# Kernel optimization log

Measured on AMD Instinct MI355X. Metric: run time of the kernel, lower is better.

The kernel has to match this reference:

```python
import jax, jax.numpy as jnp
import numpy as np

EMB_DIM = 1024
NUM_HEADS = 16
HEAD_DIM = EMB_DIM // NUM_HEADS


def setup_inputs() -> dict:
    key = jax.random.key(0)
    ks = jax.random.split(key, 10)
    B, Sq, Skv = 4, 4096, 4096
    scale = 1.0 / np.sqrt(EMB_DIM)
    inp = {
        "query": jax.random.normal(ks[0], (B, Sq, EMB_DIM), jnp.float32),
        "key_value": jax.random.normal(ks[1], (B, Skv, EMB_DIM), jnp.float32),
        "Wq": jax.random.normal(ks[2], (EMB_DIM, EMB_DIM), jnp.float32) * scale,
        "bq": jnp.zeros((EMB_DIM,), jnp.float32),
        "Wk": jax.random.normal(ks[3], (EMB_DIM, EMB_DIM), jnp.float32) * scale,
        "bk": jnp.zeros((EMB_DIM,), jnp.float32),
        "Wv": jax.random.normal(ks[4], (EMB_DIM, EMB_DIM), jnp.float32) * scale,
        "bv": jnp.zeros((EMB_DIM,), jnp.float32),
        "Wo": jax.random.normal(ks[5], (EMB_DIM, EMB_DIM), jnp.float32) * scale,
        "bo": jnp.zeros((EMB_DIM,), jnp.float32),
    }
    return inp


def reference(query, key_value, Wq, bq, Wk, bk, Wv, bv, Wo, bo):
    B, Sq, D = query.shape
    Skv = key_value.shape[1]
    H, hd = NUM_HEADS, HEAD_DIM
    # Projections -> [B, S, H, hd]
    Q = (query @ Wq + bq).reshape(B, Sq, H, hd)
    K = (key_value @ Wk + bk).reshape(B, Skv, H, hd)
    V = (key_value @ Wv + bv).reshape(B, Skv, H, hd)
    # elu+1 feature map (strictly positive)
    Q = jax.nn.elu(Q) + 1.0
    K = jax.nn.elu(K) + 1.0
    # KV summarization: [B, H, hd, hd]
    KV = jnp.einsum("bshd,bshe->bhde", K, V)
    K_sum = K.sum(axis=1)  # [B, H, hd]
    # Attention output and normalizer
    out = jnp.einsum("bqhd,bhde->bqhe", Q, KV)          # [B, Sq, H, hd]
    norm = jnp.einsum("bqhd,bhd->bqh", Q, K_sum)         # [B, Sq, H]
    out = out / (norm[..., None] + 1e-6)
    out = out.reshape(B, Sq, D)
    return out @ Wo + bo  # dropout is identity in eval
```

## Files before the change

kernel.cpp:

```cpp
#include <hip/hip_runtime.h>

typedef __bf16 bf16_t;
typedef __bf16 bf16x2 __attribute__((ext_vector_type(2)));
typedef __bf16 bf16x8 __attribute__((ext_vector_type(8)));
typedef float floatx4 __attribute__((ext_vector_type(4)));

#define B_ 4
#define S_ 4096
#define D_ 1024
#define H_ 16
#define HD_ 64
#define M_TOT (B_ * S_)

#define BM 128
#define BN 128
#define BK 64

__device__ __forceinline__ void async_load16(const bf16_t* g, bf16_t* l) {
  __builtin_amdgcn_global_load_lds(
      (const __attribute__((address_space(1))) void*)g,
      (__attribute__((address_space(3))) void*)l,
      16, 0, 0);
}

__global__ __launch_bounds__(256) void cast_kernel(const float* __restrict__ in,
                                                   bf16_t* __restrict__ out, int n) {
  int i = (blockIdx.x * 256 + threadIdx.x) * 8;
  if (i + 8 <= n) {
    float4 a = *(const float4*)(in + i);
    float4 b = *(const float4*)(in + i + 4);
    bf16x8 o;
    o[0] = (bf16_t)a.x; o[1] = (bf16_t)a.y; o[2] = (bf16_t)a.z; o[3] = (bf16_t)a.w;
    o[4] = (bf16_t)b.x; o[5] = (bf16_t)b.y; o[6] = (bf16_t)b.z; o[7] = (bf16_t)b.w;
    *(bf16x8*)(out + i) = o;
  }
}

struct WPtrs {
  const float* w0; const float* w1; const float* w2; const float* w3;
  bf16_t* t0; bf16_t* t1; bf16_t* t2; bf16_t* t3;
};

__global__ __launch_bounds__(256) void transpose_cast4_kernel(WPtrs p) {
  __shared__ float tile[32][33];
  int z = blockIdx.z;
  const float* W = z == 0 ? p.w0 : z == 1 ? p.w1 : z == 2 ? p.w2 : p.w3;
  bf16_t* Wt = z == 0 ? p.t0 : z == 1 ? p.t1 : z == 2 ? p.t2 : p.t3;
  int n0 = blockIdx.x * 32;
  int k0 = blockIdx.y * 32;
  int tx = threadIdx.x & 31;
  int ty = threadIdx.x >> 5;
  for (int r = ty; r < 32; r += 8)
    tile[r][tx] = W[(size_t)(k0 + r) * D_ + n0 + tx];
  __syncthreads();
  for (int r = ty; r < 32; r += 8)
    Wt[(size_t)(n0 + r) * D_ + k0 + tx] = (bf16_t)tile[tx][r];
}

__global__ __launch_bounds__(256) void gemm_bt_kernel(
    const bf16_t* __restrict__ A,
    const bf16_t* __restrict__ Bt,
    const float* __restrict__ bias,
    const float* __restrict__ bias2,
    bf16_t* __restrict__ outb,
    bf16_t* __restrict__ outb2,
    float* __restrict__ outf,
    int M, int N, int K, int mode) {
  __shared__ __attribute__((aligned(16))) bf16_t As[BM * BK];
  __shared__ __attribute__((aligned(16))) bf16_t Bs[BN * BK];
  const int t = threadIdx.x;
  const int w = t >> 6;
  const int lane = t & 63;

  const int L = blockIdx.y * gridDim.x + blockIdx.x;
  const int nxl2 = 31 - __clz(gridDim.x);
  const int xcd = L & 7;
  const int slot = L >> 3;
  const int mt = xcd * (gridDim.y >> 3) + (slot >> nxl2);
  const int nt = slot & ((1 << nxl2) - 1);
  const int row0 = mt * BM;
  const int col0 = nt * BN;

  const int wm = (w & 1) * 64;
  const int wn = (w >> 1) * 64;
  const int lr = lane & 15;
  const int lq = lane >> 4;
  const int rx = lr & 7;

  floatx4 acc[4][4];
#pragma unroll
  for (int i = 0; i < 4; ++i)
#pragma unroll
    for (int j = 0; j < 4; ++j) acc[i][j] = (floatx4){0.f, 0.f, 0.f, 0.f};

  for (int kt = 0; kt < K; kt += BK) {
#pragma unroll
    for (int j = 0; j < 4; ++j) {
      int s = j * 256 + t;
      int r = s >> 3;
      int cs = (((s & 7) ^ (r & 7)) << 3);
      async_load16(&A[(size_t)(row0 + r) * K + kt + cs], &As[j * 2048 + w * 512]);
      async_load16(&Bt[(size_t)(col0 + r) * K + kt + cs], &Bs[j * 2048 + w * 512]);
    }
    __syncthreads();
#pragma unroll
    for (int ks = 0; ks < BK; ks += 32) {
      const int go = ((lq + (ks >> 3)) ^ rx) << 3;
      bf16x8 af[4], bfr[4];
#pragma unroll
      for (int i = 0; i < 4; ++i)
        af[i] = *(const bf16x8*)&As[(wm + i * 16 + lr) * BK + go];
#pragma unroll
      for (int j = 0; j < 4; ++j)
        bfr[j] = *(const bf16x8*)&Bs[(wn + j * 16 + lr) * BK + go];
#pragma unroll
      for (int i = 0; i < 4; ++i)
#pragma unroll
        for (int j = 0; j < 4; ++j)
          acc[i][j] = __builtin_amdgcn_mfma_f32_16x16x32_bf16(af[i], bfr[j], acc[i][j], 0, 0, 0);
    }
    __syncthreads();
  }

#pragma unroll
  for (int i = 0; i < 4; ++i) {
#pragma unroll
    for (int j = 0; j < 4; ++j) {
      int gr = row0 + wm + i * 16 + lq * 4;
      int gc = col0 + wn + j * 16 + lr;
      if (mode == 3) {
        if (gc < 1024) {
          float bsv = bias[gc];
#pragma unroll
          for (int r = 0; r < 4; ++r) {
            float v = acc[i][j][r] + bsv;
            v = v > 0.f ? v + 1.f : __expf(v);
            outb[(size_t)(gr + r) * 1024 + gc] = (bf16_t)v;
          }
        } else {
          float bsv = bias2[gc - 1024];
#pragma unroll
          for (int r = 0; r < 4; ++r) {
            float v = acc[i][j][r] + bsv;
            outb2[(size_t)(gr + r) * 1024 + (gc - 1024)] = (bf16_t)v;
          }
        }
      } else {
        float bsv = bias[gc];
#pragma unroll
        for (int r = 0; r < 4; ++r) {
          float v = acc[i][j][r] + bsv;
          if (mode == 1) v = v > 0.f ? v + 1.f : __expf(v);
          if (mode == 2)
            outf[(size_t)(gr + r) * N + gc] = v;
          else
            outb[(size_t)(gr + r) * N + gc] = (bf16_t)v;
        }
      }
    }
  }
}

#define KVP 68
__global__ __launch_bounds__(256) void kv_mfma_kernel(
    const bf16_t* __restrict__ Kf, const bf16_t* __restrict__ Vf,
    float* __restrict__ KVtg, float* __restrict__ Ksumg) {
  __shared__ __attribute__((aligned(16))) bf16_t Kt[64 * KVP];
  __shared__ __attribute__((aligned(16))) bf16_t Vt[64 * KVP];
  const int t = threadIdx.x;
  const int w = t >> 6, lane = t & 63;
  const int lr = lane & 15, lq = lane >> 4;
  const int bh = blockIdx.x, sc = blockIdx.y;
  const int b = bh >> 4, h = bh & 15;
  const size_t base = (size_t)b * S_ * D_ + (size_t)h * HD_;
  const int p = t >> 3;
  const int c0 = (t & 7) * 8;

  floatx4 acc[4], accn[4];
#pragma unroll
  for (int j = 0; j < 4; ++j) {
    acc[j] = (floatx4){0.f, 0.f, 0.f, 0.f};
    accn[j] = (floatx4){0.f, 0.f, 0.f, 0.f};
  }
  bf16x8 ones;
#pragma unroll
  for (int u = 0; u < 8; ++u) ones[u] = (bf16_t)(lr == 0 ? 1.f : 0.f);

  for (int st = 0; st < 8; ++st) {
    int s0 = sc * 512 + st * 64;
    bf16x8 ka = *(const bf16x8*)&Kf[base + (size_t)(s0 + 2 * p) * D_ + c0];
    bf16x8 kb = *(const bf16x8*)&Kf[base + (size_t)(s0 + 2 * p + 1) * D_ + c0];
    bf16x8 va = *(const bf16x8*)&Vf[base + (size_t)(s0 + 2 * p) * D_ + c0];
    bf16x8 vb = *(const bf16x8*)&Vf[base + (size_t)(s0 + 2 * p + 1) * D_ + c0];
    __syncthreads();
#pragma unroll
    for (int u = 0; u < 8; ++u) {
      *(bf16x2*)&Kt[(c0 + u) * KVP + 2 * p] = (bf16x2){ka[u], kb[u]};
      *(bf16x2*)&Vt[(c0 + u) * KVP + 2 * p] = (bf16x2){va[u], vb[u]};
    }
    __syncthreads();
#pragma unroll
    for (int ks = 0; ks < 2; ++ks) {
      bf16x8 af = *(const bf16x8*)&Vt[(w * 16 + lr) * KVP + ks * 32 + lq * 8];
      bf16x8 bf_[4];
#pragma unroll
      for (int j = 0; j < 4; ++j)
        bf_[j] = *(const bf16x8*)&Kt[(j * 16 + lr) * KVP + ks * 32 + lq * 8];
#pragma unroll
      for (int j = 0; j < 4; ++j)
        acc[j] = __builtin_amdgcn_mfma_f32_16x16x32_bf16(af, bf_[j], acc[j], 0, 0, 0);
      if (w == 0) {
#pragma unroll
        for (int j = 0; j < 4; ++j)
          accn[j] = __builtin_amdgcn_mfma_f32_16x16x32_bf16(ones, bf_[j], accn[j], 0, 0, 0);
      }
    }
  }
  float* kvp = KVtg + (size_t)bh * 4096;
#pragma unroll
  for (int j = 0; j < 4; ++j)
#pragma unroll
    for (int r = 0; r < 4; ++r)
      atomicAdd(&kvp[(w * 16 + lq * 4 + r) * 64 + j * 16 + lr], acc[j][r]);
  if (w == 0 && lq == 0) {
#pragma unroll
    for (int j = 0; j < 4; ++j)
      atomicAdd(&Ksumg[bh * 64 + j * 16 + lr], accn[j][0]);
  }
}

__global__ __launch_bounds__(256) void attend_mfma_kernel(
    const bf16_t* __restrict__ Qf, const float* __restrict__ KVtg,
    const float* __restrict__ Ksumg, bf16_t* __restrict__ X) {
  __shared__ __attribute__((aligned(16))) bf16_t As[256 * 64];
  __shared__ __attribute__((aligned(16))) bf16_t Bs[64 * 64];
  const int t = threadIdx.x;
  const int w = t >> 6;
  const int lane = t & 63;
  const int lr = lane & 15;
  const int lq = lane >> 4;
  const int rx = lr & 7;
  const int bh = blockIdx.y;
  const int b = bh >> 4, h = bh & 15;
  const int q0 = blockIdx.x * 256;
  const size_t qbase = ((size_t)b * S_ + q0) * D_ + (size_t)h * HD_;

  {
    const int r8 = lane >> 3;
    const int cs = (((lane & 7) ^ (r8 & 7)) << 3);
#pragma unroll
    for (int it = 0; it < 8; ++it) {
      int r = w * 64 + it * 8 + r8;
      async_load16(&Qf[qbase + (size_t)r * D_ + cs], &As[(w * 64 + it * 8) * 64]);
    }
  }
  {
    const float* src = KVtg + (size_t)bh * 4096;
    int i0 = t * 16;
    float4 f0 = *(const float4*)(src + i0);
    float4 f1 = *(const float4*)(src + i0 + 4);
    float4 f2 = *(const float4*)(src + i0 + 8);
    float4 f3 = *(const float4*)(src + i0 + 12);
    bf16x8 o1, o2;
    o1[0] = (bf16_t)f0.x; o1[1] = (bf16_t)f0.y; o1[2] = (bf16_t)f0.z; o1[3] = (bf16_t)f0.w;
    o1[4] = (bf16_t)f1.x; o1[5] = (bf16_t)f1.y; o1[6] = (bf16_t)f1.z; o1[7] = (bf16_t)f1.w;
    o2[0] = (bf16_t)f2.x; o2[1] = (bf16_t)f2.y; o2[2] = (bf16_t)f2.z; o2[3] = (bf16_t)f2.w;
    o2[4] = (bf16_t)f3.x; o2[5] = (bf16_t)f3.y; o2[6] = (bf16_t)f3.z; o2[7] = (bf16_t)f3.w;
    int r = t >> 2;
    int cc = (t & 3) * 2;
    int rxw = r & 7;
    *(bf16x8*)&Bs[r * 64 + ((cc ^ rxw) << 3)] = o1;
    *(bf16x8*)&Bs[r * 64 + (((cc + 1) ^ rxw) << 3)] = o2;
  }

  bf16x8 bn[2];
#pragma unroll
  for (int ks = 0; ks < 2; ++ks) {
    bf16x8 z;
#pragma unroll
    for (int u = 0; u < 8; ++u) z[u] = (bf16_t)0.f;
    if (lr == 0) {
      const float* kp = &Ksumg[bh * 64 + ks * 32 + lq * 8];
      float4 k1 = *(const float4*)kp;
      float4 k2 = *(const float4*)(kp + 4);
      z[0] = (bf16_t)k1.x; z[1] = (bf16_t)k1.y; z[2] = (bf16_t)k1.z; z[3] = (bf16_t)k1.w;
      z[4] = (bf16_t)k2.x; z[5] = (bf16_t)k2.y; z[6] = (bf16_t)k2.z; z[7] = (bf16_t)k2.w;
    }
    bn[ks] = z;
  }

  floatx4 acc[4][4];
  floatx4 accn[4];
#pragma unroll
  for (int i = 0; i < 4; ++i) {
    accn[i] = (floatx4){0.f, 0.f, 0.f, 0.f};
#pragma unroll
    for (int j = 0; j < 4; ++j) acc[i][j] = (floatx4){0.f, 0.f, 0.f, 0.f};
  }

  __syncthreads();

#pragma unroll
  for (int ks = 0; ks < 2; ++ks) {
    const int go = ((lq + ks * 4) ^ rx) << 3;
    bf16x8 af[4], bfr[4];
#pragma unroll
    for (int i = 0; i < 4; ++i)
      af[i] = *(const bf16x8*)&As[(w * 64 + i * 16 + lr) * 64 + go];
#pragma unroll
    for (int j = 0; j < 4; ++j)
      bfr[j] = *(const bf16x8*)&Bs[(j * 16 + lr) * 64 + go];
#pragma unroll
    for (int i = 0; i < 4; ++i) {
#pragma unroll
      for (int j = 0; j < 4; ++j)
        acc[i][j] = __builtin_amdgcn_mfma_f32_16x16x32_bf16(af[i], bfr[j], acc[i][j], 0, 0, 0);
      accn[i] = __builtin_amdgcn_mfma_f32_16x16x32_bf16(af[i], bn[ks], accn[i], 0, 0, 0);
    }
  }

#pragma unroll
  for (int i = 0; i < 4; ++i) {
    int rowb = q0 + w * 64 + i * 16 + lq * 4;
#pragma unroll
    for (int r = 0; r < 4; ++r) {
      float nr = __shfl(accn[i][r], lane & 48);
      float inv = 1.f / (nr + 1e-6f);
      size_t rb = ((size_t)b * S_ + rowb + r) * D_ + (size_t)h * HD_;
#pragma unroll
      for (int j = 0; j < 4; ++j)
        X[rb + j * 16 + lr] = (bf16_t)(acc[i][j][r] * inv);
    }
  }
}

extern "C" void kernel_launch(void* const* d_in, const int* in_sizes, int n_in,
                              void* d_out, int out_size, void* d_ws, size_t ws_size,
                              hipStream_t stream) {
  const float* query     = (const float*)d_in[0];
  const float* key_value = (const float*)d_in[1];
  const float* Wq = (const float*)d_in[2];
  const float* bq = (const float*)d_in[3];
  const float* Wk = (const float*)d_in[4];
  const float* bk = (const float*)d_in[5];
  const float* Wv = (const float*)d_in[6];
  const float* bv = (const float*)d_in[7];
  const float* Wo = (const float*)d_in[8];
  const float* bo = (const float*)d_in[9];
  float* out = (float*)d_out;

  char* ws = (char*)d_ws;
  const size_t MB = 1024 * 1024;
  bf16_t* Aq   = (bf16_t*)(ws + 0);
  bf16_t* Akv  = (bf16_t*)(ws + 32 * MB);
  bf16_t* WqT  = (bf16_t*)(ws + 64 * MB);
  bf16_t* WkT  = (bf16_t*)(ws + 66 * MB);
  bf16_t* WvT  = (bf16_t*)(ws + 68 * MB);
  bf16_t* WoT  = (bf16_t*)(ws + 70 * MB);
  bf16_t* Qf   = (bf16_t*)(ws + 72 * MB);
  bf16_t* Kf   = (bf16_t*)(ws + 104 * MB);
  bf16_t* Vf   = (bf16_t*)(ws + 136 * MB);
  float*  KVtg = (float*)(ws + 168 * MB);
  float*  Ksumg= (float*)(ws + 169 * MB);

  const int NACT = M_TOT * D_;

  cast_kernel<<<NACT / 2048, 256, 0, stream>>>(query, Aq, NACT);
  cast_kernel<<<NACT / 2048, 256, 0, stream>>>(key_value, Akv, NACT);

  WPtrs wp = {Wq, Wk, Wv, Wo, WqT, WkT, WvT, WoT};
  dim3 tgrid(32, 32, 4);
  transpose_cast4_kernel<<<tgrid, 256, 0, stream>>>(wp);

  dim3 ggrid(D_ / BN, M_TOT / BM);
  dim3 ggrid2(2 * D_ / BN, M_TOT / BM);

  gemm_bt_kernel<<<ggrid, 256, 0, stream>>>(Aq, WqT, bq, nullptr, Qf, nullptr, nullptr,
                                            M_TOT, D_, D_, 1);
  gemm_bt_kernel<<<ggrid2, 256, 0, stream>>>(Akv, WkT, bk, bv, Kf, Vf, nullptr,
                                             M_TOT, 2 * D_, D_, 3);

  hipMemsetAsync(KVtg, 0, 64 * 64 * 64 * sizeof(float) + 64 * 64 * sizeof(float), stream);
  dim3 kvgrid(64, 8);
  kv_mfma_kernel<<<kvgrid, 256, 0, stream>>>(Kf, Vf, KVtg, Ksumg);

  dim3 agrid(S_ / 256, 64);
  attend_mfma_kernel<<<agrid, 256, 0, stream>>>(Qf, KVtg, Ksumg, Aq );

  gemm_bt_kernel<<<ggrid, 256, 0, stream>>>(Aq, WoT, bo, nullptr, nullptr, nullptr, out,
                                            M_TOT, D_, D_, 2);
}
```

Before: 419.3 us.

## Merge prep casts/transposes/memset into one launch and fuse Q and KV projections

Combines the two activation casts, the weight transpose-cast, and the KV accumulator zeroing into a single prep kernel. The Q projection and the fused K/V projection become one 3072-block GEMM launch with per-block selection of inputs. The output GEMM becomes a specialised kernel with compile-time dimensions and no mode branching. The aim is to cut launch count and tail idle time between small kernels, at the cost of branchy block roles and hard-coded grid sizes.

```diff
diff --git a/kernel.cpp b/kernel.cpp
--- a/kernel.cpp
+++ b/kernel.cpp
@@ -23,63 +23,73 @@
       16, 0, 0);
 }
 
-__global__ __launch_bounds__(256) void cast_kernel(const float* __restrict__ in,
-                                                   bf16_t* __restrict__ out, int n) {
-  int i = (blockIdx.x * 256 + threadIdx.x) * 8;
-  if (i + 8 <= n) {
+struct PrepArgs {
+  const float* q; const float* kv;
+  bf16_t* aq; bf16_t* akv;
+  const float* w0; const float* w1; const float* w2; const float* w3;
+  bf16_t* t0; bf16_t* t1; bf16_t* t2; bf16_t* t3;
+  float* zbase;
+};
+
+__global__ __launch_bounds__(256) void prep_kernel(PrepArgs p) {
+  __shared__ float tile[32][33];
+  const int bid = blockIdx.x;
+  const int t = threadIdx.x;
+  if (bid < 16384) {
+    const float* in = bid < 8192 ? p.q : p.kv;
+    bf16_t* out = bid < 8192 ? p.aq : p.akv;
+    int i = ((bid & 8191) * 256 + t) * 8;
     float4 a = *(const float4*)(in + i);
     float4 b = *(const float4*)(in + i + 4);
     bf16x8 o;
     o[0] = (bf16_t)a.x; o[1] = (bf16_t)a.y; o[2] = (bf16_t)a.z; o[3] = (bf16_t)a.w;
     o[4] = (bf16_t)b.x; o[5] = (bf16_t)b.y; o[6] = (bf16_t)b.z; o[7] = (bf16_t)b.w;
     *(bf16x8*)(out + i) = o;
-  }
-}
-
-struct WPtrs {
-  const float* w0; const float* w1; const float* w2; const float* w3;
-  bf16_t* t0; bf16_t* t1; bf16_t* t2; bf16_t* t3;
+  } else if (bid < 20480) {
+    int idx = bid - 16384;
+    int z = idx >> 10;
+    int rem = idx & 1023;
+    const float* W = z == 0 ? p.w0 : z == 1 ? p.w1 : z == 2 ? p.w2 : p.w3;
+    bf16_t* Wt = z == 0 ? p.t0 : z == 1 ? p.t1 : z == 2 ? p.t2 : p.t3;
+    int n0 = (rem & 31) * 32;
+    int k0 = (rem >> 5) * 32;
+    int tx = t & 31;
+    int ty = t >> 5;
+    for (int r = ty; r < 32; r += 8)
+      tile[r][tx] = W[(size_t)(k0 + r) * D_ + n0 + tx];
+    __syncthreads();
+    for (int r = ty; r < 32; r += 8)
+      Wt[(size_t)(n0 + r) * D_ + k0 + tx] = (bf16_t)tile[tx][r];
+  } else {
+    int idx = bid - 20480;
+    ((float4*)p.zbase)[idx * 256 + t] = (float4){0.f, 0.f, 0.f, 0.f};
+  }
+}
+
+struct ProjArgs {
+  const bf16_t* Aq; const bf16_t* Akv;
+  const bf16_t* WqT; const bf16_t* WkvT;
+  const float* bq; const float* bk; const float* bv;
+  bf16_t* Qf; bf16_t* Kf; bf16_t* Vf;
 };
 
-__global__ __launch_bounds__(256) void transpose_cast4_kernel(WPtrs p) {
-  __shared__ float tile[32][33];
-  int z = blockIdx.z;
-  const float* W = z == 0 ? p.w0 : z == 1 ? p.w1 : z == 2 ? p.w2 : p.w3;
-  bf16_t* Wt = z == 0 ? p.t0 : z == 1 ? p.t1 : z == 2 ? p.t2 : p.t3;
-  int n0 = blockIdx.x * 32;
-  int k0 = blockIdx.y * 32;
-  int tx = threadIdx.x & 31;
-  int ty = threadIdx.x >> 5;
-  for (int r = ty; r < 32; r += 8)
-    tile[r][tx] = W[(size_t)(k0 + r) * D_ + n0 + tx];
-  __syncthreads();
-  for (int r = ty; r < 32; r += 8)
-    Wt[(size_t)(n0 + r) * D_ + k0 + tx] = (bf16_t)tile[tx][r];
-}
-
-__global__ __launch_bounds__(256) void gemm_bt_kernel(
-    const bf16_t* __restrict__ A,
-    const bf16_t* __restrict__ Bt,
-    const float* __restrict__ bias,
-    const float* __restrict__ bias2,
-    bf16_t* __restrict__ outb,
-    bf16_t* __restrict__ outb2,
-    float* __restrict__ outf,
-    int M, int N, int K, int mode) {
+__global__ __launch_bounds__(256) void proj_kernel(ProjArgs p) {
   __shared__ __attribute__((aligned(16))) bf16_t As[BM * BK];
   __shared__ __attribute__((aligned(16))) bf16_t Bs[BN * BK];
   const int t = threadIdx.x;
   const int w = t >> 6;
   const int lane = t & 63;
 
-  const int L = blockIdx.y * gridDim.x + blockIdx.x;
-  const int nxl2 = 31 - __clz(gridDim.x);
-  const int xcd = L & 7;
-  const int slot = L >> 3;
-  const int mt = xcd * (gridDim.y >> 3) + (slot >> nxl2);
-  const int nt = slot & ((1 << nxl2) - 1);
+  const unsigned L = blockIdx.x;
+  const unsigned xcd = L & 7;
+  const unsigned slot = L >> 3;
+  const unsigned mt = xcd * 16 + slot / 24u;
+  const unsigned nt = slot % 24u;
   const int row0 = mt * BM;
-  const int col0 = nt * BN;
+  const bool isQ = nt < 8;
+  const bf16_t* A  = isQ ? p.Aq : p.Akv;
+  const bf16_t* Bt = isQ ? p.WqT : p.WkvT;
+  const int col0 = (isQ ? nt : nt - 8) * BN;
 
   const int wm = (w & 1) * 64;
   const int wn = (w >> 1) * 64;
@@ -93,14 +103,14 @@
 #pragma unroll
     for (int j = 0; j < 4; ++j) acc[i][j] = (floatx4){0.f, 0.f, 0.f, 0.f};
 
-  for (int kt = 0; kt < K; kt += BK) {
+  for (int kt = 0; kt < D_; kt += BK) {
 #pragma unroll
     for (int j = 0; j < 4; ++j) {
       int s = j * 256 + t;
       int r = s >> 3;
       int cs = (((s & 7) ^ (r & 7)) << 3);
-      async_load16(&A[(size_t)(row0 + r) * K + kt + cs], &As[j * 2048 + w * 512]);
-      async_load16(&Bt[(size_t)(col0 + r) * K + kt + cs], &Bs[j * 2048 + w * 512]);
+      async_load16(&A[(size_t)(row0 + r) * D_ + kt + cs], &As[j * 2048 + w * 512]);
+      async_load16(&Bt[(size_t)(col0 + r) * D_ + kt + cs], &Bs[j * 2048 + w * 512]);
     }
     __syncthreads();
 #pragma unroll
@@ -128,35 +138,104 @@
     for (int j = 0; j < 4; ++j) {
       int gr = row0 + wm + i * 16 + lq * 4;
       int gc = col0 + wn + j * 16 + lr;
-      if (mode == 3) {
-        if (gc < 1024) {
-          float bsv = bias[gc];
-#pragma unroll
-          for (int r = 0; r < 4; ++r) {
-            float v = acc[i][j][r] + bsv;
-            v = v > 0.f ? v + 1.f : __expf(v);
-            outb[(size_t)(gr + r) * 1024 + gc] = (bf16_t)v;
-          }
-        } else {
-          float bsv = bias2[gc - 1024];
-#pragma unroll
-          for (int r = 0; r < 4; ++r) {
-            float v = acc[i][j][r] + bsv;
-            outb2[(size_t)(gr + r) * 1024 + (gc - 1024)] = (bf16_t)v;
-          }
+      if (isQ) {
+        float bsv = p.bq[gc];
+#pragma unroll
+        for (int r = 0; r < 4; ++r) {
+          float v = acc[i][j][r] + bsv;
+          v = v > 0.f ? v + 1.f : __expf(v);
+          p.Qf[(size_t)(gr + r) * 1024 + gc] = (bf16_t)v;
+        }
+      } else if (gc < 1024) {
+        float bsv = p.bk[gc];
+#pragma unroll
+        for (int r = 0; r < 4; ++r) {
+          float v = acc[i][j][r] + bsv;
+          v = v > 0.f ? v + 1.f : __expf(v);
+          p.Kf[(size_t)(gr + r) * 1024 + gc] = (bf16_t)v;
         }
       } else {
-        float bsv = bias[gc];
+        float bsv = p.bv[gc - 1024];
 #pragma unroll
         for (int r = 0; r < 4; ++r) {
           float v = acc[i][j][r] + bsv;
-          if (mode == 1) v = v > 0.f ? v + 1.f : __expf(v);
-          if (mode == 2)
-            outf[(size_t)(gr + r) * N + gc] = v;
-          else
-            outb[(size_t)(gr + r) * N + gc] = (bf16_t)v;
+          p.Vf[(size_t)(gr + r) * 1024 + (gc - 1024)] = (bf16_t)v;
         }
       }
+    }
+  }
+}
+
+__global__ __launch_bounds__(256) void gemm_out_kernel(
+    const bf16_t* __restrict__ A,
+    const bf16_t* __restrict__ Bt,
+    const float* __restrict__ bias,
+    float* __restrict__ outf) {
+  __shared__ __attribute__((aligned(16))) bf16_t As[BM * BK];
+  __shared__ __attribute__((aligned(16))) bf16_t Bs[BN * BK];
+  const int t = threadIdx.x;
+  const int w = t >> 6;
+  const int lane = t & 63;
+
+  const int L = blockIdx.y * gridDim.x + blockIdx.x;
+  const int xcd = L & 7;
+  const int slot = L >> 3;
+  const int mt = xcd * 16 + (slot >> 3);
+  const int nt = slot & 7;
+  const int row0 = mt * BM;
+  const int col0 = nt * BN;
+
+  const int wm = (w & 1) * 64;
+  const int wn = (w >> 1) * 64;
+  const int lr = lane & 15;
+  const int lq = lane >> 4;
+  const int rx = lr & 7;
+
+  floatx4 acc[4][4];
+#pragma unroll
+  for (int i = 0; i < 4; ++i)
+#pragma unroll
+    for (int j = 0; j < 4; ++j) acc[i][j] = (floatx4){0.f, 0.f, 0.f, 0.f};
+
+  for (int kt = 0; kt < D_; kt += BK) {
+#pragma unroll
+    for (int j = 0; j < 4; ++j) {
+      int s = j * 256 + t;
+      int r = s >> 3;
+      int cs = (((s & 7) ^ (r & 7)) << 3);
+      async_load16(&A[(size_t)(row0 + r) * D_ + kt + cs], &As[j * 2048 + w * 512]);
+      async_load16(&Bt[(size_t)(col0 + r) * D_ + kt + cs], &Bs[j * 2048 + w * 512]);
+    }
+    __syncthreads();
+#pragma unroll
+    for (int ks = 0; ks < BK; ks += 32) {
+      const int go = ((lq + (ks >> 3)) ^ rx) << 3;
+      bf16x8 af[4], bfr[4];
+#pragma unroll
+      for (int i = 0; i < 4; ++i)
+        af[i] = *(const bf16x8*)&As[(wm + i * 16 + lr) * BK + go];
+#pragma unroll
+      for (int j = 0; j < 4; ++j)
+        bfr[j] = *(const bf16x8*)&Bs[(wn + j * 16 + lr) * BK + go];
+#pragma unroll
+      for (int i = 0; i < 4; ++i)
+#pragma unroll
+        for (int j = 0; j < 4; ++j)
+          acc[i][j] = __builtin_amdgcn_mfma_f32_16x16x32_bf16(af[i], bfr[j], acc[i][j], 0, 0, 0);
+    }
+    __syncthreads();
+  }
+
+#pragma unroll
+  for (int i = 0; i < 4; ++i) {
+#pragma unroll
+    for (int j = 0; j < 4; ++j) {
+      int gr = row0 + wm + i * 16 + lq * 4;
+      int gc = col0 + wn + j * 16 + lr;
+      float bsv = bias[gc];
+#pragma unroll
+      for (int r = 0; r < 4; ++r)
+        outf[(size_t)(gr + r) * D_ + gc] = acc[i][j][r] + bsv;
     }
   }
 }
@@ -363,30 +442,18 @@
   float*  KVtg = (float*)(ws + 168 * MB);
   float*  Ksumg= (float*)(ws + 169 * MB);
 
-  const int NACT = M_TOT * D_;
-
-  cast_kernel<<<NACT / 2048, 256, 0, stream>>>(query, Aq, NACT);
-  cast_kernel<<<NACT / 2048, 256, 0, stream>>>(key_value, Akv, NACT);
-
-  WPtrs wp = {Wq, Wk, Wv, Wo, WqT, WkT, WvT, WoT};
-  dim3 tgrid(32, 32, 4);
-  transpose_cast4_kernel<<<tgrid, 256, 0, stream>>>(wp);
-
-  dim3 ggrid(D_ / BN, M_TOT / BM);
-  dim3 ggrid2(2 * D_ / BN, M_TOT / BM);
-
-  gemm_bt_kernel<<<ggrid, 256, 0, stream>>>(Aq, WqT, bq, nullptr, Qf, nullptr, nullptr,
-                                            M_TOT, D_, D_, 1);
-  gemm_bt_kernel<<<ggrid2, 256, 0, stream>>>(Akv, WkT, bk, bv, Kf, Vf, nullptr,
-                                             M_TOT, 2 * D_, D_, 3);
-
-  hipMemsetAsync(KVtg, 0, 64 * 64 * 64 * sizeof(float) + 64 * 64 * sizeof(float), stream);
+  PrepArgs pa = {query, key_value, Aq, Akv, Wq, Wk, Wv, Wo, WqT, WkT, WvT, WoT, KVtg};
+  prep_kernel<<<20740, 256, 0, stream>>>(pa);
+
+  ProjArgs pj = {Aq, Akv, WqT, WkT, bq, bk, bv, Qf, Kf, Vf};
+  proj_kernel<<<3072, 256, 0, stream>>>(pj);
+
   dim3 kvgrid(64, 8);
   kv_mfma_kernel<<<kvgrid, 256, 0, stream>>>(Kf, Vf, KVtg, Ksumg);
 
   dim3 agrid(S_ / 256, 64);
   attend_mfma_kernel<<<agrid, 256, 0, stream>>>(Qf, KVtg, Ksumg, Aq );
 
-  gemm_bt_kernel<<<ggrid, 256, 0, stream>>>(Aq, WoT, bo, nullptr, nullptr, nullptr, out,
-                                            M_TOT, D_, D_, 2);
-}
+  dim3 ggrid(D_ / BN, M_TOT / BM);
+  gemm_out_kernel<<<ggrid, 256, 0, stream>>>(Aq, WoT, bo, out);
+}
```

Measured after the change: 410.5 us. 1.02x faster.
